# Kernel tuning notes

Measured on AMD Instinct MI355X. Metric: run time of the kernel, lower is better.

The kernel has to match this reference:

```python
import jax, jax.numpy as jnp
import numpy as np

N, E, D = 10000, 160000, 512


def setup_inputs() -> dict:
    key = jax.random.key(0)
    ks = jax.random.split(key, 5)
    x = jax.random.normal(ks[0], (N, D), dtype=jnp.float32)
    edge_index = jax.random.randint(ks[1], (2, E), 0, N, dtype=jnp.int32)
    W = jax.random.normal(ks[2], (D, D), dtype=jnp.float32) * (1.0 / np.sqrt(D))
    a_src = jax.random.normal(ks[3], (D,), dtype=jnp.float32) * 0.1
    a_dst = jax.random.normal(ks[4], (D,), dtype=jnp.float32) * 0.1
    bias = jnp.zeros((D,), dtype=jnp.float32)
    return {"x": x, "edge_index": edge_index, "W": W,
            "a_src": a_src, "a_dst": a_dst, "bias": bias}


def reference(x, edge_index, W, a_src, a_dst, bias):
    n = x.shape[0]
    # PyG GATConv default: add self-loops
    loops = jnp.arange(n, dtype=edge_index.dtype)
    src = jnp.concatenate([edge_index[0], loops])  # [E+N]
    dst = jnp.concatenate([edge_index[1], loops])  # [E+N]

    h = x @ W.T                                    # [N, D] linear projection
    e_src = h @ a_src                              # [N]
    e_dst = h @ a_dst                              # [N]
    e = e_src[src] + e_dst[dst]                    # [E+N]
    neg_slope = 0.2
    e = jnp.where(e > 0, e, neg_slope * e)         # leaky_relu

    # per-destination softmax (stable); self-loops guarantee non-empty segments
    m = jax.ops.segment_max(e, dst, num_segments=n)
    e = jnp.exp(e - m[dst])
    s = jax.ops.segment_sum(e, dst, num_segments=n)
    alpha = e / s[dst]                             # [E+N]

    msg = alpha[:, None] * h[src]                  # [E+N, D]
    out = jax.ops.segment_sum(msg, dst, num_segments=n) + bias  # [N, D]

    # module forward: x + elu(gat(x, edge_index))
    return x + jax.nn.elu(out)
```

## Files before the change

### kernel.cpp

```cpp
#include <hip/hip_runtime.h>
#include <hip/hip_bf16.h>

using bf16x8 = __attribute__((ext_vector_type(8))) __bf16;
using f32x4  = __attribute__((ext_vector_type(4))) float;

#define DFEAT 512
#define SLOTS 64

static __device__ __forceinline__ unsigned short f2bfbits(float f) {
    union { float f; unsigned int u; } v; v.f = f;
    unsigned int u = v.u;
    unsigned int r = (u + 0x7fffu + ((u >> 16) & 1u)) >> 16;
    return (unsigned short)r;
}

__global__ __launch_bounds__(256) void cvt_scatter_kernel(
    const float* __restrict__ x, const float* __restrict__ w,
    unsigned short* __restrict__ Xb, unsigned short* __restrict__ Wb,
    const int* __restrict__ srcv, const int* __restrict__ dstv,
    int* __restrict__ cur, int* __restrict__ slot,
    int nx4, int ntot4, int E, int T)
{
    int i = blockIdx.x * 256 + threadIdx.x;
    if (i < ntot4) {
        const float* in = (i < nx4) ? x : w;
        unsigned short* o = (i < nx4) ? Xb : Wb;
        int j = (i < nx4) ? i : i - nx4;
        float4 v = ((const float4*)in)[j];
        ushort4 u;
        u.x = f2bfbits(v.x); u.y = f2bfbits(v.y);
        u.z = f2bfbits(v.z); u.w = f2bfbits(v.w);
        ((ushort4*)o)[j] = u;
    }
    if (i < T) {
        int s, d;
        if (i < E) { s = srcv[i]; d = dstv[i]; }
        else       { s = d = i - E; }
        int pos = atomicAdd(&cur[d], 1);
        if (pos < SLOTS) slot[(size_t)d * SLOTS + pos] = s;
    }
}

__global__ __launch_bounds__(256, 2) void gemm_h_kernel(
    const unsigned short* __restrict__ X, const unsigned short* __restrict__ Wm,
    const float* __restrict__ avs, const float* __restrict__ avd,
    unsigned short* __restrict__ H, float* __restrict__ es, float* __restrict__ ed,
    int N)
{
    __shared__ unsigned short Bl[64 * 512];

    int L = blockIdx.x;
    int xcd = L & 7;
    int j   = L >> 3;
    int rpan = (j >> 3) * 8 + xcd;
    int cpan = j & 7;
    int rowPanels = (N + 127) >> 7;
    if (rpan >= rowPanels) return;
    int bm = rpan * 128;
    int bn = cpan * 64;

    int tid  = threadIdx.x;
    int wave = tid >> 6;
    int lane = tid & 63;
    int l15  = lane & 15;
    int quad = lane >> 4;

    for (int idx = tid; idx < 64 * 64; idx += 256) {
        int n = idx >> 6, c = idx & 63;
        uint4 v = *(const uint4*)(Wm + (size_t)(bn + n) * DFEAT + c * 8);
        int cs = c ^ (n & 7);
        *(uint4*)((char*)Bl + (size_t)n * 1024 + cs * 16) = v;
    }
    __syncthreads();

    int r0 = bm + wave * 32 + l15;
    int r1 = r0 + 16;
    int ra0 = r0 < N ? r0 : N - 1;
    int ra1 = r1 < N ? r1 : N - 1;
    const bf16x8* A0 = (const bf16x8*)(X + (size_t)ra0 * DFEAT);
    const bf16x8* A1 = (const bf16x8*)(X + (size_t)ra1 * DFEAT);
    const char* Bc = (const char*)Bl;
    int xorm = l15 & 7;
    int roff0 = (0 * 16 + l15) * 1024;
    int roff1 = (1 * 16 + l15) * 1024;
    int roff2 = (2 * 16 + l15) * 1024;
    int roff3 = (3 * 16 + l15) * 1024;

    f32x4 acc[2][4] = {};

    bf16x8 a0c = A0[quad],     a1c = A1[quad];
    bf16x8 a0n = A0[4 + quad], a1n = A1[4 + quad];
    bf16x8 b[4];
    {
        int cb = ((quad ^ xorm) * 16);
        b[0] = *(const bf16x8*)(Bc + roff0 + cb);
        b[1] = *(const bf16x8*)(Bc + roff1 + cb);
        b[2] = *(const bf16x8*)(Bc + roff2 + cb);
        b[3] = *(const bf16x8*)(Bc + roff3 + cb);
    }

    for (int k0 = 0; k0 < 16; ++k0) {
        int ka = ((k0 + 2 < 16 ? k0 + 2 : 15) * 4) + quad;
        bf16x8 a0f = A0[ka];
        bf16x8 a1f = A1[ka];
        int kb = ((k0 + 1 < 16 ? k0 + 1 : 15) * 4) + quad;
        int cb = (kb ^ xorm) * 16;
        bf16x8 bn0 = *(const bf16x8*)(Bc + roff0 + cb);
        bf16x8 bn1 = *(const bf16x8*)(Bc + roff1 + cb);
        bf16x8 bn2 = *(const bf16x8*)(Bc + roff2 + cb);
        bf16x8 bn3 = *(const bf16x8*)(Bc + roff3 + cb);
        acc[0][0] = __builtin_amdgcn_mfma_f32_16x16x32_bf16(a0c, b[0], acc[0][0], 0, 0, 0);
        acc[1][0] = __builtin_amdgcn_mfma_f32_16x16x32_bf16(a1c, b[0], acc[1][0], 0, 0, 0);
        acc[0][1] = __builtin_amdgcn_mfma_f32_16x16x32_bf16(a0c, b[1], acc[0][1], 0, 0, 0);
        acc[1][1] = __builtin_amdgcn_mfma_f32_16x16x32_bf16(a1c, b[1], acc[1][1], 0, 0, 0);
        acc[0][2] = __builtin_amdgcn_mfma_f32_16x16x32_bf16(a0c, b[2], acc[0][2], 0, 0, 0);
        acc[1][2] = __builtin_amdgcn_mfma_f32_16x16x32_bf16(a1c, b[2], acc[1][2], 0, 0, 0);
        acc[0][3] = __builtin_amdgcn_mfma_f32_16x16x32_bf16(a0c, b[3], acc[0][3], 0, 0, 0);
        acc[1][3] = __builtin_amdgcn_mfma_f32_16x16x32_bf16(a1c, b[3], acc[1][3], 0, 0, 0);
        a0c = a0n; a1c = a1n; a0n = a0f; a1n = a1f;
        b[0] = bn0; b[1] = bn1; b[2] = bn2; b[3] = bn3;
    }

    float as[4], ad[4];
    #pragma unroll
    for (int nt = 0; nt < 4; ++nt) {
        as[nt] = avs[bn + nt * 16 + l15];
        ad[nt] = avd[bn + nt * 16 + l15];
    }

    #pragma unroll
    for (int mt = 0; mt < 2; ++mt) {
        int rbase = bm + wave * 32 + mt * 16 + quad * 4;
        #pragma unroll
        for (int nt = 0; nt < 4; ++nt) {
            int col = bn + nt * 16 + l15;
            #pragma unroll
            for (int r = 0; r < 4; ++r) {
                int row = rbase + r;
                if (row < N) H[(size_t)row * DFEAT + col] = f2bfbits(acc[mt][nt][r]);
            }
        }
        #pragma unroll
        for (int r = 0; r < 4; ++r) {
            float ps = acc[mt][0][r] * as[0] + acc[mt][1][r] * as[1]
                     + acc[mt][2][r] * as[2] + acc[mt][3][r] * as[3];
            float pd = acc[mt][0][r] * ad[0] + acc[mt][1][r] * ad[1]
                     + acc[mt][2][r] * ad[2] + acc[mt][3][r] * ad[3];
            #pragma unroll
            for (int m = 1; m < 16; m <<= 1) {
                ps += __shfl_xor(ps, m);
                pd += __shfl_xor(pd, m);
            }
            int row = rbase + r;
            if (l15 == 0 && row < N) {
                atomicAdd(&es[row], ps);
                atomicAdd(&ed[row], pd);
            }
        }
    }
}

__global__ __launch_bounds__(256) void aggregate_kernel(
    const unsigned short* __restrict__ H, const float* __restrict__ x,
    const float* __restrict__ bias,
    const int* __restrict__ cur, const int* __restrict__ slot,
    const float* __restrict__ es, const float* __restrict__ ed,
    float* __restrict__ out, int N)
{
    int node = (blockIdx.x * 256 + threadIdx.x) >> 6;
    int lane = threadIdx.x & 63;
    if (node >= N) return;

    int k = cur[node];
    if (k > SLOTS) k = SLOTS;

    int   s = 0;
    float w = 0.f;
    if (lane < k) {
        s = slot[(size_t)node * SLOTS + lane];
        float e = es[s] + ed[node];
        e = e > 0.f ? e : 0.2f * e;
        w = __expf(e);
    }
    float denom = w;
    #pragma unroll
    for (int off = 32; off > 0; off >>= 1) denom += __shfl_xor(denom, off);
    float inv = 1.0f / denom;

    float a[8] = {};
    const unsigned short* Hl = H + lane * 8;

    auto accum = [&](int sj, float wj) {
        uint4 hv = *(const uint4*)(Hl + (size_t)sj * DFEAT);
        a[0] += wj * __uint_as_float(hv.x << 16);
        a[1] += wj * __uint_as_float(hv.x & 0xffff0000u);
        a[2] += wj * __uint_as_float(hv.y << 16);
        a[3] += wj * __uint_as_float(hv.y & 0xffff0000u);
        a[4] += wj * __uint_as_float(hv.z << 16);
        a[5] += wj * __uint_as_float(hv.z & 0xffff0000u);
        a[6] += wj * __uint_as_float(hv.w << 16);
        a[7] += wj * __uint_as_float(hv.w & 0xffff0000u);
    };

    int j = 0;
    for (; j + 3 < k; j += 4) {
        int   s0 = __shfl(s, j),     s1 = __shfl(s, j + 1);
        int   s2 = __shfl(s, j + 2), s3 = __shfl(s, j + 3);
        float w0 = __shfl(w, j),     w1 = __shfl(w, j + 1);
        float w2 = __shfl(w, j + 2), w3 = __shfl(w, j + 3);
        uint4 h0 = *(const uint4*)(Hl + (size_t)s0 * DFEAT);
        uint4 h1 = *(const uint4*)(Hl + (size_t)s1 * DFEAT);
        uint4 h2 = *(const uint4*)(Hl + (size_t)s2 * DFEAT);
        uint4 h3 = *(const uint4*)(Hl + (size_t)s3 * DFEAT);
        a[0] += w0 * __uint_as_float(h0.x << 16);
        a[1] += w0 * __uint_as_float(h0.x & 0xffff0000u);
        a[2] += w0 * __uint_as_float(h0.y << 16);
        a[3] += w0 * __uint_as_float(h0.y & 0xffff0000u);
        a[4] += w0 * __uint_as_float(h0.z << 16);
        a[5] += w0 * __uint_as_float(h0.z & 0xffff0000u);
        a[6] += w0 * __uint_as_float(h0.w << 16);
        a[7] += w0 * __uint_as_float(h0.w & 0xffff0000u);
        a[0] += w1 * __uint_as_float(h1.x << 16);
        a[1] += w1 * __uint_as_float(h1.x & 0xffff0000u);
        a[2] += w1 * __uint_as_float(h1.y << 16);
        a[3] += w1 * __uint_as_float(h1.y & 0xffff0000u);
        a[4] += w1 * __uint_as_float(h1.z << 16);
        a[5] += w1 * __uint_as_float(h1.z & 0xffff0000u);
        a[6] += w1 * __uint_as_float(h1.w << 16);
        a[7] += w1 * __uint_as_float(h1.w & 0xffff0000u);
        a[0] += w2 * __uint_as_float(h2.x << 16);
        a[1] += w2 * __uint_as_float(h2.x & 0xffff0000u);
        a[2] += w2 * __uint_as_float(h2.y << 16);
        a[3] += w2 * __uint_as_float(h2.y & 0xffff0000u);
        a[4] += w2 * __uint_as_float(h2.z << 16);
        a[5] += w2 * __uint_as_float(h2.z & 0xffff0000u);
        a[6] += w2 * __uint_as_float(h2.w << 16);
        a[7] += w2 * __uint_as_float(h2.w & 0xffff0000u);
        a[0] += w3 * __uint_as_float(h3.x << 16);
        a[1] += w3 * __uint_as_float(h3.x & 0xffff0000u);
        a[2] += w3 * __uint_as_float(h3.y << 16);
        a[3] += w3 * __uint_as_float(h3.y & 0xffff0000u);
        a[4] += w3 * __uint_as_float(h3.z << 16);
        a[5] += w3 * __uint_as_float(h3.z & 0xffff0000u);
        a[6] += w3 * __uint_as_float(h3.w << 16);
        a[7] += w3 * __uint_as_float(h3.w & 0xffff0000u);
    }
    for (; j < k; ++j) accum(__shfl(s, j), __shfl(w, j));

    int c = lane * 8;
    float4 b0 = *(const float4*)(bias + c);
    float4 b1 = *(const float4*)(bias + c + 4);
    float4 x0 = *(const float4*)(x + (size_t)node * DFEAT + c);
    float4 x1 = *(const float4*)(x + (size_t)node * DFEAT + c + 4);
    float r[8];
    r[0] = a[0] * inv + b0.x; r[1] = a[1] * inv + b0.y;
    r[2] = a[2] * inv + b0.z; r[3] = a[3] * inv + b0.w;
    r[4] = a[4] * inv + b1.x; r[5] = a[5] * inv + b1.y;
    r[6] = a[6] * inv + b1.z; r[7] = a[7] * inv + b1.w;
    #pragma unroll
    for (int i = 0; i < 8; ++i)
        r[i] = r[i] > 0.f ? r[i] : __expf(r[i]) - 1.f;
    float4 o0 = make_float4(x0.x + r[0], x0.y + r[1], x0.z + r[2], x0.w + r[3]);
    float4 o1 = make_float4(x1.x + r[4], x1.y + r[5], x1.z + r[6], x1.w + r[7]);
    *(float4*)(out + (size_t)node * DFEAT + c)     = o0;
    *(float4*)(out + (size_t)node * DFEAT + c + 4) = o1;
}

extern "C" void kernel_launch(void* const* d_in, const int* in_sizes, int n_in,
                              void* d_out, int out_size, void* d_ws, size_t ws_size,
                              hipStream_t stream)
{
    const float* x    = (const float*)d_in[0];
    const int*   edge = (const int*)d_in[1];
    const float* Wm   = (const float*)d_in[2];
    const float* avs  = (const float*)d_in[3];
    const float* avd  = (const float*)d_in[4];
    const float* bias = (const float*)d_in[5];

    const int D = DFEAT;
    const int N = in_sizes[0] / D;
    const int E = in_sizes[1] / 2;
    const int T = E + N;
    const int* srcv = edge;
    const int* dstv = edge + E;

    char* ws = (char*)d_ws;
    size_t off = 0;
    auto alloc = [&](size_t bytes) -> char* {
        char* p = ws + off;
        off += (bytes + 255) & ~(size_t)255;
        return p;
    };
    int*   cur  = (int*)alloc((size_t)N * 3 * 4);
    float* es   = (float*)(cur + N);
    float* ed   = es + N;
    int*   slot = (int*)alloc((size_t)N * SLOTS * 4);
    unsigned short* Xb = (unsigned short*)alloc((size_t)N * D * 2);
    unsigned short* Wb = (unsigned short*)alloc((size_t)D * D * 2);
    unsigned short* H  = (unsigned short*)alloc((size_t)N * D * 2);

    hipMemsetAsync(cur, 0, (size_t)N * 3 * 4, stream);

    int nx4   = (N * D) / 4;
    int ntot4 = nx4 + (D * D) / 4;
    int grid0 = (ntot4 > T ? ntot4 : T);
    cvt_scatter_kernel<<<dim3((grid0 + 255) / 256), 256, 0, stream>>>(
        x, Wm, Xb, Wb, srcv, dstv, cur, slot, nx4, ntot4, E, T);

    int rowPanels  = (N + 127) / 128;
    int rowPanels8 = ((rowPanels + 7) / 8) * 8;
    gemm_h_kernel<<<dim3(rowPanels8 * 8), 256, 0, stream>>>(
        Xb, Wb, avs, avd, H, es, ed, N);
    aggregate_kernel<<<dim3((N * 64 + 255) / 256), 256, 0, stream>>>(
        H, x, bias, cur, slot, es, ed, (float*)d_out, N);
}
```

Measured before the change: 144.2 us.

## Fuse bf16 conversion and edge scatter into GEMM kernel, deepen gather unroll

Removes the separate conversion/scatter kernel. The GEMM now reads fp32 X and W directly and converts them to bf16 in registers, and it runs the edge slot scatter as a grid-stride loop at the start of each block. The aggregate kernel batches 8 neighbor row loads before accumulating, to raise memory-level parallelism. The goal is to cut one launch and the round trip of bf16 copies through memory, at the cost of twice the A-operand global traffic in the GEMM and extra VGPR pressure.

```diff
diff --git a/kernel.cpp b/kernel.cpp
--- a/kernel.cpp
+++ b/kernel.cpp
@@ -14,40 +14,36 @@
     return (unsigned short)r;
 }
 
-__global__ __launch_bounds__(256) void cvt_scatter_kernel(
-    const float* __restrict__ x, const float* __restrict__ w,
-    unsigned short* __restrict__ Xb, unsigned short* __restrict__ Wb,
+static __device__ __forceinline__ bf16x8 cvt8(float4 lo, float4 hi) {
+    union { __hip_bfloat162 h2[4]; bf16x8 v; } u;
+    u.h2[0] = __float22bfloat162_rn(make_float2(lo.x, lo.y));
+    u.h2[1] = __float22bfloat162_rn(make_float2(lo.z, lo.w));
+    u.h2[2] = __float22bfloat162_rn(make_float2(hi.x, hi.y));
+    u.h2[3] = __float22bfloat162_rn(make_float2(hi.z, hi.w));
+    return u.v;
+}
+
+__global__ __launch_bounds__(256, 2) void gemm_h_kernel(
+    const float* __restrict__ X, const float* __restrict__ Wm,
     const int* __restrict__ srcv, const int* __restrict__ dstv,
-    int* __restrict__ cur, int* __restrict__ slot,
-    int nx4, int ntot4, int E, int T)
-{
-    int i = blockIdx.x * 256 + threadIdx.x;
-    if (i < ntot4) {
-        const float* in = (i < nx4) ? x : w;
-        unsigned short* o = (i < nx4) ? Xb : Wb;
-        int j = (i < nx4) ? i : i - nx4;
-        float4 v = ((const float4*)in)[j];
-        ushort4 u;
-        u.x = f2bfbits(v.x); u.y = f2bfbits(v.y);
-        u.z = f2bfbits(v.z); u.w = f2bfbits(v.w);
-        ((ushort4*)o)[j] = u;
-    }
-    if (i < T) {
-        int s, d;
-        if (i < E) { s = srcv[i]; d = dstv[i]; }
-        else       { s = d = i - E; }
-        int pos = atomicAdd(&cur[d], 1);
-        if (pos < SLOTS) slot[(size_t)d * SLOTS + pos] = s;
-    }
-}
-
-__global__ __launch_bounds__(256, 2) void gemm_h_kernel(
-    const unsigned short* __restrict__ X, const unsigned short* __restrict__ Wm,
     const float* __restrict__ avs, const float* __restrict__ avd,
     unsigned short* __restrict__ H, float* __restrict__ es, float* __restrict__ ed,
-    int N)
+    int* __restrict__ cur, int* __restrict__ slot,
+    int N, int E, int nBlocks)
 {
     __shared__ unsigned short Bl[64 * 512];
+
+    {
+        int T = E + N;
+        int stride = nBlocks * 256;
+        for (int i = blockIdx.x * 256 + threadIdx.x; i < T; i += stride) {
+            int s, d;
+            if (i < E) { s = srcv[i]; d = dstv[i]; }
+            else       { s = d = i - E; }
+            int pos = atomicAdd(&cur[d], 1);
+            if (pos < SLOTS) slot[(size_t)d * SLOTS + pos] = s;
+        }
+    }
 
     int L = blockIdx.x;
     int xcd = L & 7;
@@ -67,9 +63,10 @@
 
     for (int idx = tid; idx < 64 * 64; idx += 256) {
         int n = idx >> 6, c = idx & 63;
-        uint4 v = *(const uint4*)(Wm + (size_t)(bn + n) * DFEAT + c * 8);
+        const float4* wp = (const float4*)(Wm + (size_t)(bn + n) * DFEAT + c * 8);
+        bf16x8 v = cvt8(wp[0], wp[1]);
         int cs = c ^ (n & 7);
-        *(uint4*)((char*)Bl + (size_t)n * 1024 + cs * 16) = v;
+        *(bf16x8*)((char*)Bl + (size_t)n * 1024 + cs * 16) = v;
     }
     __syncthreads();
 
@@ -77,8 +74,8 @@
     int r1 = r0 + 16;
     int ra0 = r0 < N ? r0 : N - 1;
     int ra1 = r1 < N ? r1 : N - 1;
-    const bf16x8* A0 = (const bf16x8*)(X + (size_t)ra0 * DFEAT);
-    const bf16x8* A1 = (const bf16x8*)(X + (size_t)ra1 * DFEAT);
+    const float4* A0 = (const float4*)(X + (size_t)ra0 * DFEAT);
+    const float4* A1 = (const float4*)(X + (size_t)ra1 * DFEAT);
     const char* Bc = (const char*)Bl;
     int xorm = l15 & 7;
     int roff0 = (0 * 16 + l15) * 1024;
@@ -88,11 +85,14 @@
 
     f32x4 acc[2][4] = {};
 
-    bf16x8 a0c = A0[quad],     a1c = A1[quad];
-    bf16x8 a0n = A0[4 + quad], a1n = A1[4 + quad];
+    float4 a0lo_c = A0[2 * quad],     a0hi_c = A0[2 * quad + 1];
+    float4 a1lo_c = A1[2 * quad],     a1hi_c = A1[2 * quad + 1];
+    int k1 = (4 + quad) * 2;
+    float4 a0lo_n = A0[k1], a0hi_n = A0[k1 + 1];
+    float4 a1lo_n = A1[k1], a1hi_n = A1[k1 + 1];
     bf16x8 b[4];
     {
-        int cb = ((quad ^ xorm) * 16);
+        int cb = (quad ^ xorm) * 16;
         b[0] = *(const bf16x8*)(Bc + roff0 + cb);
         b[1] = *(const bf16x8*)(Bc + roff1 + cb);
         b[2] = *(const bf16x8*)(Bc + roff2 + cb);
@@ -100,24 +100,27 @@
     }
 
     for (int k0 = 0; k0 < 16; ++k0) {
-        int ka = ((k0 + 2 < 16 ? k0 + 2 : 15) * 4) + quad;
-        bf16x8 a0f = A0[ka];
-        bf16x8 a1f = A1[ka];
+        int ka = ((k0 + 2 < 16 ? k0 + 2 : 15) * 4 + quad) * 2;
+        float4 f0lo = A0[ka], f0hi = A0[ka + 1];
+        float4 f1lo = A1[ka], f1hi = A1[ka + 1];
         int kb = ((k0 + 1 < 16 ? k0 + 1 : 15) * 4) + quad;
         int cb = (kb ^ xorm) * 16;
         bf16x8 bn0 = *(const bf16x8*)(Bc + roff0 + cb);
         bf16x8 bn1 = *(const bf16x8*)(Bc + roff1 + cb);
         bf16x8 bn2 = *(const bf16x8*)(Bc + roff2 + cb);
         bf16x8 bn3 = *(const bf16x8*)(Bc + roff3 + cb);
-        acc[0][0] = __builtin_amdgcn_mfma_f32_16x16x32_bf16(a0c, b[0], acc[0][0], 0, 0, 0);
-        acc[1][0] = __builtin_amdgcn_mfma_f32_16x16x32_bf16(a1c, b[0], acc[1][0], 0, 0, 0);
-        acc[0][1] = __builtin_amdgcn_mfma_f32_16x16x32_bf16(a0c, b[1], acc[0][1], 0, 0, 0);
-        acc[1][1] = __builtin_amdgcn_mfma_f32_16x16x32_bf16(a1c, b[1], acc[1][1], 0, 0, 0);
-        acc[0][2] = __builtin_amdgcn_mfma_f32_16x16x32_bf16(a0c, b[2], acc[0][2], 0, 0, 0);
-        acc[1][2] = __builtin_amdgcn_mfma_f32_16x16x32_bf16(a1c, b[2], acc[1][2], 0, 0, 0);
-        acc[0][3] = __builtin_amdgcn_mfma_f32_16x16x32_bf16(a0c, b[3], acc[0][3], 0, 0, 0);
-        acc[1][3] = __builtin_amdgcn_mfma_f32_16x16x32_bf16(a1c, b[3], acc[1][3], 0, 0, 0);
-        a0c = a0n; a1c = a1n; a0n = a0f; a1n = a1f;
+        bf16x8 a0 = cvt8(a0lo_c, a0hi_c);
+        bf16x8 a1 = cvt8(a1lo_c, a1hi_c);
+        acc[0][0] = __builtin_amdgcn_mfma_f32_16x16x32_bf16(a0, b[0], acc[0][0], 0, 0, 0);
+        acc[1][0] = __builtin_amdgcn_mfma_f32_16x16x32_bf16(a1, b[0], acc[1][0], 0, 0, 0);
+        acc[0][1] = __builtin_amdgcn_mfma_f32_16x16x32_bf16(a0, b[1], acc[0][1], 0, 0, 0);
+        acc[1][1] = __builtin_amdgcn_mfma_f32_16x16x32_bf16(a1, b[1], acc[1][1], 0, 0, 0);
+        acc[0][2] = __builtin_amdgcn_mfma_f32_16x16x32_bf16(a0, b[2], acc[0][2], 0, 0, 0);
+        acc[1][2] = __builtin_amdgcn_mfma_f32_16x16x32_bf16(a1, b[2], acc[1][2], 0, 0, 0);
+        acc[0][3] = __builtin_amdgcn_mfma_f32_16x16x32_bf16(a0, b[3], acc[0][3], 0, 0, 0);
+        acc[1][3] = __builtin_amdgcn_mfma_f32_16x16x32_bf16(a1, b[3], acc[1][3], 0, 0, 0);
+        a0lo_c = a0lo_n; a0hi_c = a0hi_n; a1lo_c = a1lo_n; a1hi_c = a1hi_n;
+        a0lo_n = f0lo;   a0hi_n = f0hi;   a1lo_n = f1lo;   a1hi_n = f1hi;
         b[0] = bn0; b[1] = bn1; b[2] = bn2; b[3] = bn3;
     }
 
@@ -190,8 +193,7 @@
     float a[8] = {};
     const unsigned short* Hl = H + lane * 8;
 
-    auto accum = [&](int sj, float wj) {
-        uint4 hv = *(const uint4*)(Hl + (size_t)sj * DFEAT);
+    auto fma8 = [&](uint4 hv, float wj) {
         a[0] += wj * __uint_as_float(hv.x << 16);
         a[1] += wj * __uint_as_float(hv.x & 0xffff0000u);
         a[2] += wj * __uint_as_float(hv.y << 16);
@@ -203,49 +205,34 @@
     };
 
     int j = 0;
-    for (; j + 3 < k; j += 4) {
-        int   s0 = __shfl(s, j),     s1 = __shfl(s, j + 1);
-        int   s2 = __shfl(s, j + 2), s3 = __shfl(s, j + 3);
-        float w0 = __shfl(w, j),     w1 = __shfl(w, j + 1);
-        float w2 = __shfl(w, j + 2), w3 = __shfl(w, j + 3);
-        uint4 h0 = *(const uint4*)(Hl + (size_t)s0 * DFEAT);
-        uint4 h1 = *(const uint4*)(Hl + (size_t)s1 * DFEAT);
-        uint4 h2 = *(const uint4*)(Hl + (size_t)s2 * DFEAT);
-        uint4 h3 = *(const uint4*)(Hl + (size_t)s3 * DFEAT);
-        a[0] += w0 * __uint_as_float(h0.x << 16);
-        a[1] += w0 * __uint_as_float(h0.x & 0xffff0000u);
-        a[2] += w0 * __uint_as_float(h0.y << 16);
-        a[3] += w0 * __uint_as_float(h0.y & 0xffff0000u);
-        a[4] += w0 * __uint_as_float(h0.z << 16);
-        a[5] += w0 * __uint_as_float(h0.z & 0xffff0000u);
-        a[6] += w0 * __uint_as_float(h0.w << 16);
-        a[7] += w0 * __uint_as_float(h0.w & 0xffff0000u);
-        a[0] += w1 * __uint_as_float(h1.x << 16);
-        a[1] += w1 * __uint_as_float(h1.x & 0xffff0000u);
-        a[2] += w1 * __uint_as_float(h1.y << 16);
-        a[3] += w1 * __uint_as_float(h1.y & 0xffff0000u);
-        a[4] += w1 * __uint_as_float(h1.z << 16);
-        a[5] += w1 * __uint_as_float(h1.z & 0xffff0000u);
-        a[6] += w1 * __uint_as_float(h1.w << 16);
-        a[7] += w1 * __uint_as_float(h1.w & 0xffff0000u);
-        a[0] += w2 * __uint_as_float(h2.x << 16);
-        a[1] += w2 * __uint_as_float(h2.x & 0xffff0000u);
-        a[2] += w2 * __uint_as_float(h2.y << 16);
-        a[3] += w2 * __uint_as_float(h2.y & 0xffff0000u);
-        a[4] += w2 * __uint_as_float(h2.z << 16);
-        a[5] += w2 * __uint_as_float(h2.z & 0xffff0000u);
-        a[6] += w2 * __uint_as_float(h2.w << 16);
-        a[7] += w2 * __uint_as_float(h2.w & 0xffff0000u);
-        a[0] += w3 * __uint_as_float(h3.x << 16);
-        a[1] += w3 * __uint_as_float(h3.x & 0xffff0000u);
-        a[2] += w3 * __uint_as_float(h3.y << 16);
-        a[3] += w3 * __uint_as_float(h3.y & 0xffff0000u);
-        a[4] += w3 * __uint_as_float(h3.z << 16);
-        a[5] += w3 * __uint_as_float(h3.z & 0xffff0000u);
-        a[6] += w3 * __uint_as_float(h3.w << 16);
-        a[7] += w3 * __uint_as_float(h3.w & 0xffff0000u);
-    }
-    for (; j < k; ++j) accum(__shfl(s, j), __shfl(w, j));
+    for (; j + 7 < k; j += 8) {
+        uint4 h[8]; float wj[8];
+        #pragma unroll
+        for (int q = 0; q < 8; ++q) {
+            int   sq = __shfl(s, j + q);
+            wj[q]    = __shfl(w, j + q);
+            h[q] = *(const uint4*)(Hl + (size_t)sq * DFEAT);
+        }
+        #pragma unroll
+        for (int q = 0; q < 8; ++q) fma8(h[q], wj[q]);
+    }
+    if (j + 3 < k) {
+        uint4 h[4]; float wj[4];
+        #pragma unroll
+        for (int q = 0; q < 4; ++q) {
+            int   sq = __shfl(s, j + q);
+            wj[q]    = __shfl(w, j + q);
+            h[q] = *(const uint4*)(Hl + (size_t)sq * DFEAT);
+        }
+        #pragma unroll
+        for (int q = 0; q < 4; ++q) fma8(h[q], wj[q]);
+        j += 4;
+    }
+    for (; j < k; ++j) {
+        int   sq = __shfl(s, j);
+        float wj = __shfl(w, j);
+        fma8(*(const uint4*)(Hl + (size_t)sq * DFEAT), wj);
+    }
 
     int c = lane * 8;
     float4 b0 = *(const float4*)(bias + c);
@@ -280,7 +267,6 @@
     const int D = DFEAT;
     const int N = in_sizes[0] / D;
     const int E = in_sizes[1] / 2;
-    const int T = E + N;
     const int* srcv = edge;
     const int* dstv = edge + E;
 
@@ -295,22 +281,15 @@
     float* es   = (float*)(cur + N);
     float* ed   = es + N;
     int*   slot = (int*)alloc((size_t)N * SLOTS * 4);
-    unsigned short* Xb = (unsigned short*)alloc((size_t)N * D * 2);
-    unsigned short* Wb = (unsigned short*)alloc((size_t)D * D * 2);
-    unsigned short* H  = (unsigned short*)alloc((size_t)N * D * 2);
+    unsigned short* H = (unsigned short*)alloc((size_t)N * D * 2);
 
     hipMemsetAsync(cur, 0, (size_t)N * 3 * 4, stream);
-
-    int nx4   = (N * D) / 4;
-    int ntot4 = nx4 + (D * D) / 4;
-    int grid0 = (ntot4 > T ? ntot4 : T);
-    cvt_scatter_kernel<<<dim3((grid0 + 255) / 256), 256, 0, stream>>>(
-        x, Wm, Xb, Wb, srcv, dstv, cur, slot, nx4, ntot4, E, T);
 
     int rowPanels  = (N + 127) / 128;
     int rowPanels8 = ((rowPanels + 7) / 8) * 8;
-    gemm_h_kernel<<<dim3(rowPanels8 * 8), 256, 0, stream>>>(
-        Xb, Wb, avs, avd, H, es, ed, N);
+    int nBlocks    = rowPanels8 * 8;
+    gemm_h_kernel<<<dim3(nBlocks), 256, 0, stream>>>(
+        x, Wm, srcv, dstv, avs, avd, H, es, ed, cur, slot, N, E, nBlocks);
     aggregate_kernel<<<dim3((N * 64 + 255) / 256), 256, 0, stream>>>(
         H, x, bias, cur, slot, es, ed, (float*)d_out, N);
 }
```

New measurement: 150.8 us. 4.6% more time.
